# Performance work log

Hardware: AMD Instinct MI355X
Metric: run time of the kernel (lower is better)

The kernel has to match this reference:

```python
import jax, jax.numpy as jnp
import numpy as np

B, T = 512, 64
C_IN, C_HID, C_OUT = 512, 512, 256
SIZE_INP = C_IN + C_HID + C_OUT  # 1280
SIZE_GATES = 4 * C_HID           # 2048


def setup_inputs() -> dict:
    key = jax.random.key(0)
    k1, k2, k3, k4, k5 = jax.random.split(key, 5)
    s_rnn = 1.0 / np.sqrt(SIZE_INP)
    s_feat = 1.0 / np.sqrt(C_HID)
    return {
        "z": jax.random.normal(k1, (B, T, C_IN, 1, 1), dtype=jnp.float32),
        "r0": jnp.zeros((B, C_OUT, 1, 1), dtype=jnp.float32),
        "h0": jnp.zeros((B, C_HID, 1, 1), dtype=jnp.float32),
        "c0": jnp.zeros((B, C_HID, 1, 1), dtype=jnp.float32),
        "W_rnn": jax.random.uniform(k2, (SIZE_GATES, SIZE_INP), jnp.float32, -s_rnn, s_rnn),
        "b_rnn": jax.random.uniform(k3, (SIZE_GATES,), jnp.float32, -s_rnn, s_rnn),
        "W_feat": jax.random.uniform(k4, (C_OUT, C_HID), jnp.float32, -s_feat, s_feat),
        "b_feat": jax.random.uniform(k5, (C_OUT,), jnp.float32, -s_feat, s_feat),
    }


def reference(z, r0, h0, c0, W_rnn, b_rnn, W_feat, b_feat):
    # 1x1 convs on [B,C,1,1] tensors are plain matmuls over channels.
    zs = z[..., 0, 0]  # [B, T, C_in]

    def step(carry, z_t):
        r, h, c = carry  # [B,Cout], [B,H], [B,H]
        inp = jnp.concatenate([r, h, z_t], axis=1)          # [B, 1280]
        gates = inp @ W_rnn.T + b_rnn                       # [B, 4H]
        f, i, s, o = jnp.split(gates, 4, axis=1)            # torch.chunk order
        c_n = jax.nn.sigmoid(f) * c + jax.nn.sigmoid(i) * jnp.tanh(s)
        h_n = jax.nn.sigmoid(o) * jnp.tanh(c_n)
        r_n = r + h_n @ W_feat.T + b_feat
        return (r_n, h_n, c_n), None

    carry0 = (r0[..., 0, 0], h0[..., 0, 0], c0[..., 0, 0])
    (r, h, c), _ = jax.lax.scan(step, carry0, jnp.swapaxes(zs, 0, 1))
    return r[..., None, None], (h[..., None, None], c[..., None, None])
```

## Files before the change

kernel.cpp:

```cpp
#include <hip/hip_runtime.h>
#include <hip/hip_fp16.h>


using f32x4 = __attribute__((ext_vector_type(4))) float;
using f16x8 = __attribute__((ext_vector_type(8))) _Float16;
using fp16x2 = __attribute__((ext_vector_type(2))) __fp16;

union U4H8 { uint4 u; f16x8 h; fp16x2 p[4]; };

__device__ __forceinline__ float sigm(float x){ return 1.0f/(1.0f + __expf(-x)); }
__device__ __forceinline__ float tanhfast(float x){
  x = fminf(fmaxf(x, -30.f), 30.f);
  float e = __expf(2.0f*x);
  return (e - 1.0f)/(e + 1.0f);
}

#define MFMA16(a,b,c) __builtin_amdgcn_mfma_f32_16x16x32_f16((a).h,(b).h,(c),0,0,0)


__global__ void k_wft(const float* __restrict__ wf, float* __restrict__ wft){
  int idx = blockIdx.x*256 + threadIdx.x;
  int c = idx & 511; int j = idx >> 9;
  wft[c*256 + j] = wf[idx];
}

__global__ void k_bias2(const float* __restrict__ wrnn, const float* __restrict__ brnn,
                        const float* __restrict__ bfeat, float* __restrict__ biasp){
  int wv = (blockIdx.x*256 + threadIdx.x) >> 6;
  int lane = threadIdx.x & 63;
  int g = (wv&3)*512 + (wv>>2);
  const float* wr = wrnn + (size_t)g*1280;
  float s = 0.f;
  for (int j = lane; j < 256; j += 64) s += bfeat[j]*wr[j];
  for (int off = 32; off; off >>= 1) s += __shfl_down(s, off, 64);
  if (lane == 0) biasp[wv] = brnn[g] + s;
}

__global__ void k_whp4(const float* __restrict__ wrnn, const float* __restrict__ wft,
                       float* __restrict__ whp_part){
  int s = blockIdx.x >> 8;
  int tl = blockIdx.x & 255;
  int bn = tl & 31, bk = tl >> 5;
  __shared__ float wrs[64][37];
  __shared__ float wfs[64][37];
  int tid = threadIdx.x;
  int tn = tid & 15, tk = tid >> 4;
  float accv[4][4];
  #pragma unroll
  for (int x=0;x<4;x++) for (int y=0;y<4;y++) accv[x][y]=0.f;
  for (int jc = s*64; jc < s*64+64; jc += 32){
    __syncthreads();
    for (int idx = tid; idx < 64*32; idx += 256){
      int r = idx >> 5, j = idx & 31;
      int n = bn*64 + r; int g = (n&3)*512 + (n>>2);
      wrs[r][j] = wrnn[(size_t)g*1280 + jc + j];
      wfs[r][j] = wft[(bk*64 + r)*256 + jc + j];
    }
    __syncthreads();
    for (int j=0;j<32;j++){
      float a[4], b[4];
      #pragma unroll
      for (int x=0;x<4;x++){ a[x] = wfs[tk*4+x][j]; b[x] = wrs[tn*4+x][j]; }
      #pragma unroll
      for (int x=0;x<4;x++)
        #pragma unroll
        for (int y=0;y<4;y++) accv[x][y] += a[x]*b[y];
    }
  }
  float* dst = whp_part + (size_t)s*1048576;
  for (int x=0;x<4;x++){
    int kk = bk*64 + tk*4 + x;
    for (int y=0;y<4;y++){
      int n = bn*64 + tn*4 + y;
      dst[(size_t)kk*2048 + n] = accv[x][y];
    }
  }
}

__global__ void k_whpadd(const float* __restrict__ p, float* __restrict__ o){
  int i = (blockIdx.x*256 + threadIdx.x)*4;
  float4 a = *(const float4*)(p + i);
  float4 b = *(const float4*)(p + 1048576 + i);
  float4 c = *(const float4*)(p + 2097152 + i);
  float4 d = *(const float4*)(p + 3145728 + i);
  float4 r;
  r.x = a.x+b.x+c.x+d.x; r.y = a.y+b.y+c.y+d.y;
  r.z = a.z+b.z+c.z+d.z; r.w = a.w+b.w+c.w+d.w;
  *(float4*)(o + i) = r;
}

__global__ void k_rinit(const float* __restrict__ r0, const float* __restrict__ h0,
                        const float* __restrict__ wft, const float* __restrict__ bfeat,
                        float* __restrict__ rd32, __half* __restrict__ rd16){
  __shared__ float hs[512];
  int row = blockIdx.x; int j = threadIdx.x;
  for (int k = threadIdx.x; k < 512; k += 256) hs[k] = h0[row*512 + k];
  __syncthreads();
  float acc = 0.f;
  for (int k=0;k<512;k++) acc += hs[k]*wft[k*256 + j];
  float rr = r0[row*256 + j] - acc - bfeat[j];
  rd32[row*256 + j] = rr;
  int ridx = (((row>>4)*8 + (j>>5))*64 + (row&15) + (((j&31)>>3)<<4))*8 + (j&7);
  rd16[ridx] = __float2half(rr);
}

__global__ void k_packh0(const float* __restrict__ h0, const float* __restrict__ c0,
                         __half* __restrict__ h16, float* __restrict__ c32){
  int idx = blockIdx.x*256 + threadIdx.x;
  int e = idx & 7, l = (idx>>3) & 63, kc = (idx>>9) & 15, mt = idx >> 13;
  int row = mt*16 + (l&15);
  int k = kc*32 + ((l>>4)<<3) + e;
  h16[idx] = __float2half(h0[row*512 + k]);
  c32[idx] = c0[idx];
}

__global__ void k_pack(const float* __restrict__ wrnn, const float* __restrict__ whp32,
                       const float* __restrict__ wfeat, __half* __restrict__ dst,
                       int mode, int NT16, int KCH){
  int tot = NT16*KCH*512;
  for (int idx = blockIdx.x*256 + threadIdx.x; idx < tot; idx += gridDim.x*256){
    int e = idx & 7; int l = (idx>>3) & 63;
    int kc = (idx>>9) % KCH; int nt = (idx>>9) / KCH;
    int k = kc*32 + ((l>>4)<<3) + e;
    int n = nt*16 + (l&15);
    float v;
    if (mode == 0){
      int g = (n&3)*512 + (n>>2);
      if (k < 256) v = wrnn[(size_t)g*1280 + k];
      else         v = whp32[(size_t)(k-256)*2048 + n] + wrnn[(size_t)g*1280 + k];
    } else if (mode == 2){
      int g = (n&3)*512 + (n>>2);
      v = wrnn[(size_t)g*1280 + 768 + k];
    } else {
      v = wfeat[(size_t)n*512 + k];
    }
    dst[idx] = __float2half(v);
  }
}

__global__ void k_zpackall(const float* __restrict__ z, __half* __restrict__ z16){
  int u = blockIdx.x*256 + threadIdx.x;
  int k0 = (u & 63) * 8;
  int b4 = (u >> 6) & 127;
  int t  = u >> 13;
  int b = b4 * 4;
  int frag = (t*32 + (b>>4))*16 + (k0>>5);
  uint4 wv[4];
  #pragma unroll
  for (int j=0;j<4;j++){
    const float4* src = (const float4*)(z + ((size_t)((b+j)*64 + t))*512 + k0);
    float4 f0 = src[0], f1 = src[1];
    U4H8 a;
    a.p[0] = __builtin_amdgcn_cvt_pkrtz(f0.x, f0.y);
    a.p[1] = __builtin_amdgcn_cvt_pkrtz(f0.z, f0.w);
    a.p[2] = __builtin_amdgcn_cvt_pkrtz(f1.x, f1.y);
    a.p[3] = __builtin_amdgcn_cvt_pkrtz(f1.z, f1.w);
    wv[j] = a.u;
  }
  uint4* dst = (uint4*)z16 + (size_t)frag*64 + (b & 15) + (((k0 & 31) >> 3) << 4);
  #pragma unroll
  for (int j=0;j<4;j++) dst[j] = wv[j];
}

__global__ __launch_bounds__(512) void k_gzbig(const __half* __restrict__ z16,
    const __half* __restrict__ bpz, const float* __restrict__ biasp,
    __half* __restrict__ gz){
  const int tid = threadIdx.x, lane = tid & 63, w = tid >> 6;
  const int wr = w >> 2, wc = w & 3;
  const int xcd = blockIdx.x & 7, j = blockIdx.x >> 3;
  const int bm = xcd*32 + (j & 31);
  const int bn = j >> 5;
  const int tt = bm >> 2, bq = bm & 3;
  const int mt0 = tt*32 + bq*8 + wr*4;
  const int nt0 = bn*8 + wc*2;
  const uint4* A = (const uint4*)z16 + (size_t)(mt0*16)*64 + lane;
  const uint4* B = (const uint4*)bpz + (size_t)(nt0*16)*64 + lane;
  f32x4 acc[4][2];
  #pragma unroll
  for (int mi=0;mi<4;mi++){ acc[mi][0]=(f32x4){0,0,0,0}; acc[mi][1]=(f32x4){0,0,0,0}; }
  #pragma unroll 2
  for (int kc=0; kc<16; ++kc){
    U4H8 b0v, b1v;
    b0v.u = B[kc*64];
    b1v.u = B[(16+kc)*64];
    #pragma unroll
    for (int mi=0; mi<4; mi++){
      U4H8 a;
      a.u = A[(mi*16 + kc)*64];
      acc[mi][0] = MFMA16(a, b0v, acc[mi][0]);
      acc[mi][1] = MFMA16(a, b1v, acc[mi][1]);
    }
  }
  #pragma unroll
  for (int ns=0; ns<2; ns++){
    int n = (nt0 + ns)*16 + (lane & 15);
    float bp = biasp[n];
    #pragma unroll
    for (int mi=0; mi<4; mi++){
      #pragma unroll
      for (int i=0; i<4; i++){
        int brow = bq*128 + wr*64 + mi*16 + ((lane>>4)<<2) + i;
        gz[((size_t)(tt*512 + brow))*2048 + n] = __float2half(acc[mi][ns][i] + bp);
      }
    }
  }
}

__global__ __launch_bounds__(576) void k_stepF(
    const __half* __restrict__ rd16_in, const __half* __restrict__ h16_in,
    float* __restrict__ rd32,
    __half* __restrict__ rd16_out, __half* __restrict__ h16_out,
    float* __restrict__ c32,
    const __half* __restrict__ gz,
    const __half* __restrict__ bp_rec, const __half* __restrict__ bf_pack,
    const float* __restrict__ bfeat,
    float* __restrict__ out_h, float* __restrict__ out_c, float* __restrict__ out_r,
    int step, int mode){
  __shared__ float cls[64][69];
  const int tid = threadIdx.x, lane = tid & 63;
  const int bid = blockIdx.x;
  const int bm = (bid>>3) & 7;
  const int bn = (bid&7)*4 + (bid>>6);

  if (mode == 0 && tid < 512){
    const int w = tid >> 6, wr = w >> 2, wc = w & 3;
    f32x4 acc0 = (f32x4){0,0,0,0}, acc1 = (f32x4){0,0,0,0};
    const int mtA = bm*4 + wr*2;
    const int nt  = bn*4 + wc;
    const uint4* a0p = (const uint4*)rd16_in + (size_t)(mtA*8)*64 + lane;
    const uint4* a1p = a0p + 8*64;
    const uint4* h0p = (const uint4*)h16_in + (size_t)(mtA*16)*64 + lane;
    const uint4* h1p = h0p + 16*64;
    const uint4* bp  = (const uint4*)bp_rec + (size_t)(nt*24)*64 + lane;
    #pragma unroll 4
    for (int kc=0; kc<8; ++kc){
      U4H8 a0,a1,b;
      a0.u = a0p[kc*64]; a1.u = a1p[kc*64]; b.u = bp[kc*64];
      acc0 = MFMA16(a0,b,acc0);
      acc1 = MFMA16(a1,b,acc1);
    }
    #pragma unroll 4
    for (int kc=0; kc<16; ++kc){
      U4H8 a0,a1,b;
      a0.u = h0p[kc*64]; a1.u = h1p[kc*64]; b.u = bp[(8+kc)*64];
      acc0 = MFMA16(a0,b,acc0);
      acc1 = MFMA16(a1,b,acc1);
    }
    #pragma unroll
    for (int i=0; i<4; i++){
      cls[wr*32 +      ((lane>>4)<<2) + i][wc*16 + (lane&15)] = acc0[i];
      cls[wr*32 + 16 + ((lane>>4)<<2) + i][wc*16 + (lane&15)] = acc1[i];
    }
  } else if (tid >= 512){
    const int mt = (bid>>3) & 31;
    const int nc = bid & 7;
    f32x4 racc0 = (f32x4){0,0,0,0}, racc1 = (f32x4){0,0,0,0};
    const uint4* hp  = (const uint4*)h16_in + (size_t)(mt*16)*64 + lane;
    const uint4* bf0 = (const uint4*)bf_pack + (size_t)((nc*2)*16)*64 + lane;
    const uint4* bf1 = bf0 + 16*64;
    #pragma unroll 4
    for (int kc=0; kc<16; ++kc){
      U4H8 a,b0,b1;
      a.u = hp[kc*64]; b0.u = bf0[kc*64]; b1.u = bf1[kc*64];
      racc0 = MFMA16(a,b0,racc0);
      racc1 = MFMA16(a,b1,racc1);
    }
    #pragma unroll
    for (int ns=0; ns<2; ns++){
      const f32x4 rv = ns ? racc1 : racc0;
      const int col = (nc*2+ns)*16 + (lane&15);
      const float bfv = bfeat[col];
      #pragma unroll
      for (int i=0;i<4;i++){
        const int grow = mt*16 + ((lane>>4)<<2) + i;
        size_t x = (size_t)grow*256 + col;
        float rr = rv[i] + rd32[x] + bfv;
        if (mode == 1){
          out_r[x] = rr;
        } else {
          rd32[x] = rr;
          int ridx = (((grow>>4)*8 + (col>>5))*64
                      + (grow&15) + (((col&31)>>3)<<4))*8 + (col&7);
          rd16_out[ridx] = __float2half(rr);
        }
      }
    }
  }

  if (mode == 0){
    __syncthreads();
    if (tid < 512){
      const __half* gzt = gz + (size_t)step*1048576;
      #pragma unroll
      for (int rep=0; rep<2; rep++){
        int idx = rep*512 + tid;
        int jl = idx & 15, row = idx >> 4;
        int grow = bm*64 + row;
        int j = bn*16 + jl;
        const __half2* gp = (const __half2*)(gzt + (size_t)grow*2048 + bn*64 + jl*4);
        __half2 p0 = gp[0], p1 = gp[1];
        float g0 = cls[row][jl*4+0] + __half2float(p0.x);
        float g1 = cls[row][jl*4+1] + __half2float(p0.y);
        float g2 = cls[row][jl*4+2] + __half2float(p1.x);
        float g3 = cls[row][jl*4+3] + __half2float(p1.y);
        float cold = c32[(size_t)grow*512 + j];
        float f  = sigm(g0);
        float ii = sigm(g1);
        float s  = tanhfast(g2);
        float o  = sigm(g3);
        float cn = f*cold + ii*s;
        float hn = o*tanhfast(cn);
        c32[(size_t)grow*512 + j] = cn;
        int hidx = (((grow>>4)*16 + (j>>5))*64 + (grow&15) + (((j&31)>>3)<<4))*8 + (j&7);
        h16_out[hidx] = __float2half(hn);
        if (step == 63){
          out_h[(size_t)grow*512 + j] = hn;
          out_c[(size_t)grow*512 + j] = cn;
        }
      }
    }
  }
}

extern "C" void kernel_launch(void* const* d_in, const int* in_sizes, int n_in,
                              void* d_out, int out_size, void* d_ws, size_t ws_size,
                              hipStream_t stream){
  const float* z     = (const float*)d_in[0];
  const float* r0    = (const float*)d_in[1];
  const float* h0    = (const float*)d_in[2];
  const float* c0    = (const float*)d_in[3];
  const float* wrnn  = (const float*)d_in[4];
  const float* brnn  = (const float*)d_in[5];
  const float* wfeat = (const float*)d_in[6];
  const float* bfeat = (const float*)d_in[7];
  float* out = (float*)d_out;

  char* wsb = (char*)d_ws;
  size_t off = 0;
  auto alloc = [&](size_t bytes)->char*{
    char* p = wsb + off; off = (off + bytes + 255) & ~(size_t)255; return p;
  };
  __half* z16     = (__half*)alloc((size_t)64*512*512*2);
  __half* bp_rec  = (__half*)alloc((size_t)128*24*512*2);
  __half* bpz     = (__half*)alloc((size_t)128*16*512*2);
  __half* bf_pack = (__half*)alloc((size_t)16*16*512*2);
  float*  biasp   = (float*) alloc(2048*4);
  float*  wft32   = (float*) alloc((size_t)512*256*4);
  __half* h16A    = (__half*)alloc((size_t)512*512*2);
  __half* h16B    = (__half*)alloc((size_t)512*512*2);
  __half* rd16A   = (__half*)alloc((size_t)512*256*2);
  __half* rd16B   = (__half*)alloc((size_t)512*256*2);
  float*  rd32    = (float*) alloc((size_t)512*256*4);
  float*  c32     = (float*) alloc((size_t)512*512*4);
  __half* gz      = (__half*)alloc((size_t)64*512*2048*2);
  (void)ws_size;
  float* whp32    = (float*)gz;
  float* whp_part = (float*)gz + 1048576;

  k_wft     <<<dim3(512),  dim3(256), 0, stream>>>(wfeat, wft32);
  k_bias2   <<<dim3(512),  dim3(256), 0, stream>>>(wrnn, brnn, bfeat, biasp);
  k_whp4    <<<dim3(1024), dim3(256), 0, stream>>>(wrnn, wft32, whp_part);
  k_whpadd  <<<dim3(1024), dim3(256), 0, stream>>>(whp_part, whp32);
  k_rinit   <<<dim3(512),  dim3(256), 0, stream>>>(r0, h0, wft32, bfeat, rd32, rd16A);
  k_packh0  <<<dim3(1024), dim3(256), 0, stream>>>(h0, c0, h16A, c32);
  k_pack    <<<dim3(1024), dim3(256), 0, stream>>>(wrnn, whp32, wfeat, bp_rec, 0, 128, 24);
  k_pack    <<<dim3(1024), dim3(256), 0, stream>>>(wrnn, whp32, wfeat, bpz,    2, 128, 16);
  k_pack    <<<dim3(64),   dim3(256), 0, stream>>>(wrnn, whp32, wfeat, bf_pack,3,  16, 16);
  k_zpackall<<<dim3(2048), dim3(256), 0, stream>>>(z, z16);
  k_gzbig   <<<dim3(4096), dim3(512), 0, stream>>>(z16, bpz, biasp, gz);

  __half* h16in = h16A;  __half* h16out = h16B;
  __half* rd16in = rd16A; __half* rd16out = rd16B;
  for (int t = 1; t <= 64; ++t){
    k_stepF<<<dim3(256), dim3(576), 0, stream>>>(
        rd16in, h16in, rd32, rd16out, h16out, c32, gz,
        bp_rec, bf_pack, bfeat,
        out + 131072, out + 393216, (float*)nullptr, t-1, 0);
    __half* th;
    th = h16in; h16in = h16out; h16out = th;
    th = rd16in; rd16in = rd16out; rd16out = th;
  }
  k_stepF<<<dim3(256), dim3(576), 0, stream>>>(
      rd16in, h16in, rd32, rd16out, h16out, c32, gz,
      bp_rec, bf_pack, bfeat,
      (float*)nullptr, (float*)nullptr, out, 64, 1);
}
```

Measured before the change: 827.7 us.

## Swap MFMA operands to fuse gate epilogue in registers; restage input-projection GEMM

The step kernel now computes the recurrent gate tile with weights as the A operand. Each lane's accumulator then holds all four gates (f,i,s,o) of one hidden unit, so the LSTM cell update runs directly from registers. This removes the shared-memory staging buffer and the block-wide barrier. Grid size doubles to 512 blocks with half the per-wave tile, which raises parallelism per step but re-reads more weight fragments. The precomputed z-projection GEMM is also restructured: each block stages its A tile in 64KB of LDS and loops over all N tiles, which may change occupancy and write patterns.

```diff
diff --git a/kernel.cpp b/kernel.cpp
--- a/kernel.cpp
+++ b/kernel.cpp
@@ -7,6 +7,7 @@
 using fp16x2 = __attribute__((ext_vector_type(2))) __fp16;
 
 union U4H8 { uint4 u; f16x8 h; fp16x2 p[4]; };
+union GZU { uint2 u; __half2 h2[2]; };
 
 __device__ __forceinline__ float sigm(float x){ return 1.0f/(1.0f + __expf(-x)); }
 __device__ __forceinline__ float tanhfast(float x){
@@ -162,46 +163,42 @@
   for (int j=0;j<4;j++) dst[j] = wv[j];
 }
 
-__global__ __launch_bounds__(512) void k_gzbig(const __half* __restrict__ z16,
+__global__ __launch_bounds__(512) void k_gzbig2(const __half* __restrict__ z16,
     const __half* __restrict__ bpz, const float* __restrict__ biasp,
     __half* __restrict__ gz){
+  __shared__ __half als[32768];
   const int tid = threadIdx.x, lane = tid & 63, w = tid >> 6;
-  const int wr = w >> 2, wc = w & 3;
-  const int xcd = blockIdx.x & 7, j = blockIdx.x >> 3;
-  const int bm = xcd*32 + (j & 31);
-  const int bn = j >> 5;
-  const int tt = bm >> 2, bq = bm & 3;
-  const int mt0 = tt*32 + bq*8 + wr*4;
-  const int nt0 = bn*8 + wc*2;
-  const uint4* A = (const uint4*)z16 + (size_t)(mt0*16)*64 + lane;
-  const uint4* B = (const uint4*)bpz + (size_t)(nt0*16)*64 + lane;
-  f32x4 acc[4][2];
-  #pragma unroll
-  for (int mi=0;mi<4;mi++){ acc[mi][0]=(f32x4){0,0,0,0}; acc[mi][1]=(f32x4){0,0,0,0}; }
-  #pragma unroll 2
-  for (int kc=0; kc<16; ++kc){
-    U4H8 b0v, b1v;
-    b0v.u = B[kc*64];
-    b1v.u = B[(16+kc)*64];
+  const int bm = blockIdx.x;
+  {
+    const uint4* src = (const uint4*)z16 + (size_t)(bm*64)*64;
+    uint4* dst = (uint4*)als;
+    for (int i = tid; i < 4096; i += 512) dst[i] = src[i];
+  }
+  __syncthreads();
+  const int mtl = w >> 1;
+  const int nth = w & 1;
+  const uint4* A = (const uint4*)als + (mtl*16)*64 + lane;
+  const int row0 = (bm*4 + mtl)*16 + ((lane>>4)<<2);
+  for (int ntp = 0; ntp < 32; ++ntp){
+    const int nt = nth*64 + ntp*2;
+    const uint4* B0 = (const uint4*)bpz + (size_t)(nt*16)*64 + lane;
+    const uint4* B1 = B0 + 16*64;
+    f32x4 acc0 = (f32x4){0,0,0,0}, acc1 = (f32x4){0,0,0,0};
+    #pragma unroll 4
+    for (int kc=0; kc<16; ++kc){
+      U4H8 a,b0,b1;
+      a.u = A[kc*64]; b0.u = B0[kc*64]; b1.u = B1[kc*64];
+      acc0 = MFMA16(a,b0,acc0);
+      acc1 = MFMA16(a,b1,acc1);
+    }
     #pragma unroll
-    for (int mi=0; mi<4; mi++){
-      U4H8 a;
-      a.u = A[(mi*16 + kc)*64];
-      acc[mi][0] = MFMA16(a, b0v, acc[mi][0]);
-      acc[mi][1] = MFMA16(a, b1v, acc[mi][1]);
-    }
-  }
-  #pragma unroll
-  for (int ns=0; ns<2; ns++){
-    int n = (nt0 + ns)*16 + (lane & 15);
-    float bp = biasp[n];
-    #pragma unroll
-    for (int mi=0; mi<4; mi++){
+    for (int ns=0; ns<2; ns++){
+      const f32x4 av = ns ? acc1 : acc0;
+      const int n = (nt+ns)*16 + (lane&15);
+      const float bp = biasp[n];
       #pragma unroll
-      for (int i=0; i<4; i++){
-        int brow = bq*128 + wr*64 + mi*16 + ((lane>>4)<<2) + i;
-        gz[((size_t)(tt*512 + brow))*2048 + n] = __float2half(acc[mi][ns][i] + bp);
-      }
+      for (int i=0;i<4;i++)
+        gz[(size_t)(row0+i)*2048 + n] = __float2half(av[i] + bp);
     }
   }
 }
@@ -216,107 +213,83 @@
     const float* __restrict__ bfeat,
     float* __restrict__ out_h, float* __restrict__ out_c, float* __restrict__ out_r,
     int step, int mode){
-  __shared__ float cls[64][69];
   const int tid = threadIdx.x, lane = tid & 63;
   const int bid = blockIdx.x;
-  const int bm = (bid>>3) & 7;
-  const int bn = (bid&7)*4 + (bid>>6);
-
-  if (mode == 0 && tid < 512){
+
+  if (tid < 512){
+    if (mode == 1) return;
     const int w = tid >> 6, wr = w >> 2, wc = w & 3;
-    f32x4 acc0 = (f32x4){0,0,0,0}, acc1 = (f32x4){0,0,0,0};
-    const int mtA = bm*4 + wr*2;
+    const int u = bid >> 3;
+    const int bm = u & 15;
+    const int bn = (bid & 7)*4 + (u >> 4);
+    const int mtA = bm*2 + wr;
     const int nt  = bn*4 + wc;
-    const uint4* a0p = (const uint4*)rd16_in + (size_t)(mtA*8)*64 + lane;
-    const uint4* a1p = a0p + 8*64;
-    const uint4* h0p = (const uint4*)h16_in + (size_t)(mtA*16)*64 + lane;
-    const uint4* h1p = h0p + 16*64;
-    const uint4* bp  = (const uint4*)bp_rec + (size_t)(nt*24)*64 + lane;
+    const int batch = bm*32 + wr*16 + (lane & 15);
+    const int n0 = nt*16 + ((lane>>4)<<2);
+    const int j  = n0 >> 2;
+    const __half* gzt = gz + (size_t)step*1048576;
+    GZU gu; gu.u = *(const uint2*)(gzt + (size_t)batch*2048 + n0);
+    const float cold = c32[(size_t)batch*512 + j];
+    const uint4* ap = (const uint4*)rd16_in + (size_t)(mtA*8)*64 + lane;
+    const uint4* hp = (const uint4*)h16_in + (size_t)(mtA*16)*64 + lane;
+    const uint4* bp = (const uint4*)bp_rec + (size_t)(nt*24)*64 + lane;
+    f32x4 acc = (f32x4){0,0,0,0};
     #pragma unroll 4
     for (int kc=0; kc<8; ++kc){
-      U4H8 a0,a1,b;
-      a0.u = a0p[kc*64]; a1.u = a1p[kc*64]; b.u = bp[kc*64];
-      acc0 = MFMA16(a0,b,acc0);
-      acc1 = MFMA16(a1,b,acc1);
+      U4H8 a,b;
+      a.u = ap[kc*64]; b.u = bp[kc*64];
+      acc = MFMA16(b,a,acc);
     }
     #pragma unroll 4
     for (int kc=0; kc<16; ++kc){
-      U4H8 a0,a1,b;
-      a0.u = h0p[kc*64]; a1.u = h1p[kc*64]; b.u = bp[(8+kc)*64];
-      acc0 = MFMA16(a0,b,acc0);
-      acc1 = MFMA16(a1,b,acc1);
-    }
-    #pragma unroll
-    for (int i=0; i<4; i++){
-      cls[wr*32 +      ((lane>>4)<<2) + i][wc*16 + (lane&15)] = acc0[i];
-      cls[wr*32 + 16 + ((lane>>4)<<2) + i][wc*16 + (lane&15)] = acc1[i];
-    }
-  } else if (tid >= 512){
-    const int mt = (bid>>3) & 31;
-    const int nc = bid & 7;
-    f32x4 racc0 = (f32x4){0,0,0,0}, racc1 = (f32x4){0,0,0,0};
-    const uint4* hp  = (const uint4*)h16_in + (size_t)(mt*16)*64 + lane;
-    const uint4* bf0 = (const uint4*)bf_pack + (size_t)((nc*2)*16)*64 + lane;
-    const uint4* bf1 = bf0 + 16*64;
+      U4H8 a,b;
+      a.u = hp[kc*64]; b.u = bp[(8+kc)*64];
+      acc = MFMA16(b,a,acc);
+    }
+    const float g0 = acc[0] + __half2float(gu.h2[0].x);
+    const float g1 = acc[1] + __half2float(gu.h2[0].y);
+    const float g2 = acc[2] + __half2float(gu.h2[1].x);
+    const float g3 = acc[3] + __half2float(gu.h2[1].y);
+    const float f  = sigm(g0);
+    const float ii = sigm(g1);
+    const float s  = tanhfast(g2);
+    const float o  = sigm(g3);
+    const float cn = f*cold + ii*s;
+    const float hn = o*tanhfast(cn);
+    c32[(size_t)batch*512 + j] = cn;
+    const int hidx = (((batch>>4)*16 + (j>>5))*64
+                      + (batch&15) + (((j&31)>>3)<<4))*8 + (j&7);
+    h16_out[hidx] = __float2half(hn);
+    if (step == 63){
+      out_h[(size_t)batch*512 + j] = hn;
+      out_c[(size_t)batch*512 + j] = cn;
+    }
+  } else {
+    const int mt = bid >> 4;
+    const int nc = bid & 15;
+    const uint4* hp = (const uint4*)h16_in + (size_t)(mt*16)*64 + lane;
+    const uint4* bf = (const uint4*)bf_pack + (size_t)(nc*16)*64 + lane;
+    f32x4 racc = (f32x4){0,0,0,0};
     #pragma unroll 4
     for (int kc=0; kc<16; ++kc){
-      U4H8 a,b0,b1;
-      a.u = hp[kc*64]; b0.u = bf0[kc*64]; b1.u = bf1[kc*64];
-      racc0 = MFMA16(a,b0,racc0);
-      racc1 = MFMA16(a,b1,racc1);
-    }
+      U4H8 a,b;
+      a.u = hp[kc*64]; b.u = bf[kc*64];
+      racc = MFMA16(a,b,racc);
+    }
+    const int col = nc*16 + (lane&15);
+    const float bfv = bfeat[col];
     #pragma unroll
-    for (int ns=0; ns<2; ns++){
-      const f32x4 rv = ns ? racc1 : racc0;
-      const int col = (nc*2+ns)*16 + (lane&15);
-      const float bfv = bfeat[col];
-      #pragma unroll
-      for (int i=0;i<4;i++){
-        const int grow = mt*16 + ((lane>>4)<<2) + i;
-        size_t x = (size_t)grow*256 + col;
-        float rr = rv[i] + rd32[x] + bfv;
-        if (mode == 1){
-          out_r[x] = rr;
-        } else {
-          rd32[x] = rr;
-          int ridx = (((grow>>4)*8 + (col>>5))*64
-                      + (grow&15) + (((col&31)>>3)<<4))*8 + (col&7);
-          rd16_out[ridx] = __float2half(rr);
-        }
-      }
-    }
-  }
-
-  if (mode == 0){
-    __syncthreads();
-    if (tid < 512){
-      const __half* gzt = gz + (size_t)step*1048576;
-      #pragma unroll
-      for (int rep=0; rep<2; rep++){
-        int idx = rep*512 + tid;
-        int jl = idx & 15, row = idx >> 4;
-        int grow = bm*64 + row;
-        int j = bn*16 + jl;
-        const __half2* gp = (const __half2*)(gzt + (size_t)grow*2048 + bn*64 + jl*4);
-        __half2 p0 = gp[0], p1 = gp[1];
-        float g0 = cls[row][jl*4+0] + __half2float(p0.x);
-        float g1 = cls[row][jl*4+1] + __half2float(p0.y);
-        float g2 = cls[row][jl*4+2] + __half2float(p1.x);
-        float g3 = cls[row][jl*4+3] + __half2float(p1.y);
-        float cold = c32[(size_t)grow*512 + j];
-        float f  = sigm(g0);
-        float ii = sigm(g1);
-        float s  = tanhfast(g2);
-        float o  = sigm(g3);
-        float cn = f*cold + ii*s;
-        float hn = o*tanhfast(cn);
-        c32[(size_t)grow*512 + j] = cn;
-        int hidx = (((grow>>4)*16 + (j>>5))*64 + (grow&15) + (((j&31)>>3)<<4))*8 + (j&7);
-        h16_out[hidx] = __float2half(hn);
-        if (step == 63){
-          out_h[(size_t)grow*512 + j] = hn;
-          out_c[(size_t)grow*512 + j] = cn;
-        }
+    for (int i=0;i<4;i++){
+      const int grow = mt*16 + ((lane>>4)<<2) + i;
+      const size_t x = (size_t)grow*256 + col;
+      const float rr = racc[i] + rd32[x] + bfv;
+      if (mode == 1){
+        out_r[x] = rr;
+      } else {
+        rd32[x] = rr;
+        const int ridx = (((grow>>4)*8 + (col>>5))*64
+                          + (grow&15) + (((col&31)>>3)<<4))*8 + (col&7);
+        rd16_out[ridx] = __float2half(rr);
       }
     }
   }
@@ -367,12 +340,12 @@
   k_pack    <<<dim3(1024), dim3(256), 0, stream>>>(wrnn, whp32, wfeat, bpz,    2, 128, 16);
   k_pack    <<<dim3(64),   dim3(256), 0, stream>>>(wrnn, whp32, wfeat, bf_pack,3,  16, 16);
   k_zpackall<<<dim3(2048), dim3(256), 0, stream>>>(z, z16);
-  k_gzbig   <<<dim3(4096), dim3(512), 0, stream>>>(z16, bpz, biasp, gz);
+  k_gzbig2  <<<dim3(512),  dim3(512), 0, stream>>>(z16, bpz, biasp, gz);
 
   __half* h16in = h16A;  __half* h16out = h16B;
   __half* rd16in = rd16A; __half* rd16out = rd16B;
   for (int t = 1; t <= 64; ++t){
-    k_stepF<<<dim3(256), dim3(576), 0, stream>>>(
+    k_stepF<<<dim3(512), dim3(576), 0, stream>>>(
         rd16in, h16in, rd32, rd16out, h16out, c32, gz,
         bp_rec, bf_pack, bfeat,
         out + 131072, out + 393216, (float*)nullptr, t-1, 0);
@@ -380,7 +353,7 @@
     th = h16in; h16in = h16out; h16out = th;
     th = rd16in; rd16in = rd16out; rd16out = th;
   }
-  k_stepF<<<dim3(256), dim3(576), 0, stream>>>(
+  k_stepF<<<dim3(512), dim3(576), 0, stream>>>(
       rd16in, h16in, rd32, rd16out, h16out, c32, gz,
       bp_rec, bf_pack, bfeat,
       (float*)nullptr, (float*)nullptr, out, 64, 1);
```

After: 953.2 us. 1.15x slower.
